# Performance work log

Hardware: AMD Instinct MI355X
Metric: run time of the kernel (lower is better)

Reference implementation:

```python
import jax, jax.numpy as jnp
import numpy as np

B, S, D = 16, 1024, 1024   # batch, n_assets, d_model
H, DK = 16, 64             # num_heads, key_dim (H*DK == D)


def setup_inputs() -> dict:
    key = jax.random.key(0)
    ks = jax.random.split(key, 6)
    scale = 0.02
    return {
        "inputs": jax.random.normal(ks[0], (B, S, D), dtype=jnp.float32),
        "lead_lag_bias": jax.random.normal(ks[1], (S, S), dtype=jnp.float32),
        "Wq": jax.random.normal(ks[2], (D, H * DK), dtype=jnp.float32) * scale,
        "Wk": jax.random.normal(ks[3], (D, H * DK), dtype=jnp.float32) * scale,
        "Wv": jax.random.normal(ks[4], (D, H * DK), dtype=jnp.float32) * scale,
        "Wo": jax.random.normal(ks[5], (H * DK, D), dtype=jnp.float32) * scale,
        "bias_transform": jnp.ones((H,), dtype=jnp.float32),
    }


def reference(inputs, lead_lag_bias, Wq, Wk, Wv, Wo, bias_transform):
    # inputs: [B, S, D]; lead_lag_bias: [S, S]
    inv_sqrt_dk = 1.0 / np.sqrt(DK)
    q = (inputs @ Wq).reshape(B, S, H, DK).transpose(0, 2, 1, 3)  # [B,H,S,Dk]
    k = (inputs @ Wk).reshape(B, S, H, DK).transpose(0, 2, 1, 3)
    v = (inputs @ Wv).reshape(B, S, H, DK).transpose(0, 2, 1, 3)
    scores = jnp.einsum('bhqd,bhkd->bhqk', q, k) * inv_sqrt_dk  # [B,H,S,S]
    # per-head scaled static lead-lag bias (broadcast over batch)
    scores = scores + bias_transform[None, :, None, None] * lead_lag_bias[None, None, :, :]
    attn = jax.nn.softmax(scores, axis=-1)
    out = jnp.einsum('bhqk,bhkd->bhqd', attn, v)  # [B,H,S,Dk]
    out = out.transpose(0, 2, 1, 3).reshape(B, S, H * DK)
    return out @ Wo  # [B, S, D]
```

## Files before the change

### kernel.cpp

```cpp
#include <hip/hip_runtime.h>

typedef __attribute__((ext_vector_type(4))) float f32x4;
typedef __attribute__((ext_vector_type(8))) __bf16 bf16x8;
typedef __attribute__((ext_vector_type(8))) unsigned short u16x8;
typedef __attribute__((ext_vector_type(2))) unsigned int u32x2;

#define MFMA16(a, b, c) \
  __builtin_amdgcn_mfma_f32_16x16x32_bf16(__builtin_bit_cast(bf16x8, (a)), \
                                          __builtin_bit_cast(bf16x8, (b)), (c), 0, 0, 0)

__device__ __forceinline__ unsigned short f2bf(float f) {
  unsigned int u = __builtin_bit_cast(unsigned int, f);
  u += 0x7FFFu + ((u >> 16) & 1u);
  return (unsigned short)(u >> 16);
}

__device__ __forceinline__ unsigned int packbf(float lo, float hi) {
  return (unsigned int)f2bf(lo) | ((unsigned int)f2bf(hi) << 16);
}

__device__ __forceinline__ void gload16(const void* g, void* l) {
  __builtin_amdgcn_global_load_lds(
      (const __attribute__((address_space(1))) void*)g,
      (__attribute__((address_space(3))) void*)l, 16, 0, 0);
}

__global__ __launch_bounds__(256) void xconv(
    const float* __restrict__ X, unsigned short* __restrict__ Xb)
{
  size_t i = ((size_t)blockIdx.x * 256 + threadIdx.x) * 8;
  f32x4 f0 = *(const f32x4*)(X + i);
  f32x4 f1 = *(const f32x4*)(X + i + 4);
  u16x8 v;
  v[0] = f2bf(f0[0]); v[1] = f2bf(f0[1]); v[2] = f2bf(f0[2]); v[3] = f2bf(f0[3]);
  v[4] = f2bf(f1[0]); v[5] = f2bf(f1[1]); v[6] = f2bf(f1[2]); v[7] = f2bf(f1[3]);
  *(u16x8*)(Xb + i) = v;
}

__global__ __launch_bounds__(256) void wtrans(
    const float* __restrict__ Wq, const float* __restrict__ Wk,
    const float* __restrict__ Wv, const float* __restrict__ Wo,
    unsigned short* __restrict__ Wt)
{
  __shared__ unsigned short tile[32][33];
  const int z = blockIdx.z;
  const float* W = (z == 0) ? Wq : (z == 1) ? Wk : (z == 2) ? Wv : Wo;
  unsigned short* T = Wt + (size_t)z * 1024 * 1024;
  const int tx = threadIdx.x, ty = threadIdx.y;
  const int x = blockIdx.x * 32 + tx;
  const int y0 = blockIdx.y * 32;
#pragma unroll
  for (int i = 0; i < 4; ++i)
    tile[ty + i * 8][tx] = f2bf(W[(size_t)(y0 + ty + i * 8) * 1024 + x]);
  __syncthreads();
#pragma unroll
  for (int i = 0; i < 4; ++i)
    T[(size_t)(blockIdx.x * 32 + ty + i * 8) * 1024 + y0 + tx] = tile[tx][ty + i * 8];
}

__global__ __launch_bounds__(256) void qkv_gemm(
    const unsigned short* __restrict__ Xb, const unsigned short* __restrict__ Wt,
    unsigned short* __restrict__ Qo, unsigned short* __restrict__ Ko,
    unsigned short* __restrict__ Vo)
{
  const int bx = blockIdx.x;
  const int z = bx >> 3;
  const int bn = (bx & 7) * 128;
  const int bm = blockIdx.y * 128;
  const unsigned short* Wz = Wt + (size_t)z * 1024 * 1024;
  unsigned short* Out = (z == 0) ? Qo : (z == 1) ? Ko : Vo;

  const int tid = threadIdx.x;
  const int w = tid >> 6, l = tid & 63, l15 = l & 15, lg = l >> 4;
  const int wr = w >> 1, wc = w & 1;

  __shared__ alignas(16) unsigned short sA[128][32];
  __shared__ alignas(16) unsigned short sB[128][32];

  const int srow = w * 32 + (l >> 2);
  const int scol = (l & 3) * 8;
  const unsigned short* gA = Xb + (size_t)(bm + srow) * 1024 + scol;
  const unsigned short* gB = Wz + (size_t)(bn + srow) * 1024 + scol;
  unsigned short* lA = &sA[srow][scol];
  unsigned short* lB = &sB[srow][scol];

  f32x4 acc[4][4];
  const f32x4 zero = {0.f, 0.f, 0.f, 0.f};
#pragma unroll
  for (int i = 0; i < 4; ++i)
#pragma unroll
    for (int j = 0; j < 4; ++j) acc[i][j] = zero;

  for (int k0 = 0; k0 < 1024; k0 += 32) {
    __syncthreads();
#pragma unroll
    for (int p = 0; p < 2; ++p) {
      gload16(gA + (size_t)p * 16 * 1024 + k0, lA + p * 16 * 32);
      gload16(gB + (size_t)p * 16 * 1024 + k0, lB + p * 16 * 32);
    }
    __syncthreads();

    u16x8 af[4], bf[4];
#pragma unroll
    for (int m = 0; m < 4; ++m)
      af[m] = *(const u16x8*)&sA[wr * 64 + m * 16 + l15][lg * 8];
#pragma unroll
    for (int n = 0; n < 4; ++n)
      bf[n] = *(const u16x8*)&sB[wc * 64 + n * 16 + l15][lg * 8];
#pragma unroll
    for (int m = 0; m < 4; ++m)
#pragma unroll
      for (int n = 0; n < 4; ++n)
        acc[m][n] = MFMA16(af[m], bf[n], acc[m][n]);
  }

#pragma unroll
  for (int m = 0; m < 4; ++m) {
    int grow_b = bm + wr * 64 + m * 16 + lg * 4;
#pragma unroll
    for (int n = 0; n < 4; ++n) {
      int gcol = bn + wc * 64 + n * 16 + l15;
      int hh = gcol >> 6, dk = gcol & 63;
#pragma unroll
      for (int t = 0; t < 4; ++t) {
        int grow = grow_b + t;
        int bb = grow >> 10, s = grow & 1023;
        Out[(((size_t)(bb * 16 + hh)) * 1024 + s) * 64 + dk] = f2bf(acc[m][n][t]);
      }
    }
  }
}

__global__ __launch_bounds__(256) void vtrans(
    const unsigned short* __restrict__ V, unsigned short* __restrict__ Vt)
{
  __shared__ unsigned short tile[64 * 64];
  const int s0 = blockIdx.x * 64;
  const size_t bh = (size_t)blockIdx.y * (64 * 1024);
  const int tid = threadIdx.x;

#pragma unroll
  for (int p = 0; p < 2; ++p) {
    int id = p * 256 + tid;
    int s = id >> 3, cc = id & 7;
    u16x8 v = *(const u16x8*)(V + bh + (size_t)(s0 + s) * 64 + cc * 8);
    *(u16x8*)&tile[s * 64 + ((cc ^ (s >> 3)) * 8)] = v;
  }
  __syncthreads();
#pragma unroll
  for (int p = 0; p < 2; ++p) {
    int id = p * 256 + tid;
    int d = id >> 3, sc = id & 7;
    u16x8 v;
#pragma unroll
    for (int i = 0; i < 8; ++i)
      v[i] = tile[(sc * 8 + i) * 64 + (((d >> 3) ^ sc) * 8) + (d & 7)];
    *(u16x8*)(Vt + bh + (size_t)d * 1024 + s0 + sc * 8) = v;
  }
}

__global__ __launch_bounds__(256) void attn(
    const unsigned short* __restrict__ Q, const unsigned short* __restrict__ Kg,
    const unsigned short* __restrict__ Vtg, const float* __restrict__ LL,
    const float* __restrict__ btr, unsigned short* __restrict__ O)
{
  const int q0 = blockIdx.x * 64;
  const int h = blockIdx.y, b = blockIdx.z;
  const int tid = threadIdx.x;
  const int w = tid >> 6, l = tid & 63, l15 = l & 15, lg = l >> 4;

  __shared__ alignas(16) unsigned short sK[64 * 64];
  __shared__ alignas(16) unsigned short sVt[64 * 64];
  __shared__ alignas(16) unsigned short sP[4][16 * 64];

  const float bt = btr[h];
  const size_t bh = (size_t)(b * 16 + h) * (1024 * 64);
  const unsigned short* Qb = Q + bh;
  const unsigned short* Kp = Kg + bh;
  const unsigned short* Vp = Vtg + bh;

  u16x8 qf[2];
  {
    const unsigned short* qp = Qb + (size_t)(q0 + w * 16 + l15) * 64 + lg * 8;
    qf[0] = *(const u16x8*)qp;
    qf[1] = *(const u16x8*)(qp + 32);
  }
  const int qrow = q0 + w * 16 + l15;

  float mrow = -1e30f, lrow = 0.f;
  f32x4 o[4];
  const f32x4 zero = {0.f, 0.f, 0.f, 0.f};
#pragma unroll
  for (int dn = 0; dn < 4; ++dn) o[dn] = zero;

  const int srow0 = tid >> 3, scc = tid & 7;

  for (int kt = 0; kt < 16; ++kt) {
    __syncthreads();
#pragma unroll
    for (int p = 0; p < 2; ++p) {
      int row = p * 32 + srow0;
      u16x8 vk = *(const u16x8*)(Kp + (size_t)(kt * 64 + row) * 64 + scc * 8);
      u16x8 vv = *(const u16x8*)(Vp + (size_t)row * 1024 + kt * 64 + scc * 8);
      *(u16x8*)&sK[row * 64 + ((scc ^ (row & 7)) * 8)] = vk;
      *(u16x8*)&sVt[row * 64 + ((scc ^ (row & 7)) * 8)] = vv;
    }
    __syncthreads();

    f32x4 llv[4];
#pragma unroll
    for (int jn = 0; jn < 4; ++jn)
      llv[jn] = *(const f32x4*)(LL + (size_t)qrow * 1024 + kt * 64 + jn * 16 + lg * 4);

    f32x4 s[4];
#pragma unroll
    for (int jn = 0; jn < 4; ++jn) s[jn] = zero;
#pragma unroll
    for (int dc = 0; dc < 2; ++dc) {
#pragma unroll
      for (int jn = 0; jn < 4; ++jn) {
        int row = jn * 16 + l15;
        u16x8 kfr = *(const u16x8*)&sK[row * 64 + (((dc * 4 + lg) ^ (row & 7)) * 8)];
        s[jn] = MFMA16(kfr, qf[dc], s[jn]);
      }
    }

#pragma unroll
    for (int jn = 0; jn < 4; ++jn)
#pragma unroll
      for (int t = 0; t < 4; ++t)
        s[jn][t] = s[jn][t] * 0.125f + bt * llv[jn][t];

    float tm = s[0][0];
#pragma unroll
    for (int jn = 0; jn < 4; ++jn)
#pragma unroll
      for (int t = 0; t < 4; ++t) tm = fmaxf(tm, s[jn][t]);
    tm = fmaxf(tm, __shfl_xor(tm, 16, 64));
    tm = fmaxf(tm, __shfl_xor(tm, 32, 64));
    float mn = fmaxf(mrow, tm);
    float sc = __expf(mrow - mn);
    mrow = mn;

    float rs = 0.f;
    unsigned int pk[4][2];
#pragma unroll
    for (int jn = 0; jn < 4; ++jn) {
      float p0 = __expf(s[jn][0] - mn);
      float p1 = __expf(s[jn][1] - mn);
      float p2 = __expf(s[jn][2] - mn);
      float p3 = __expf(s[jn][3] - mn);
      rs += (p0 + p1) + (p2 + p3);
      pk[jn][0] = packbf(p0, p1);
      pk[jn][1] = packbf(p2, p3);
    }
    rs += __shfl_xor(rs, 16, 64);
    rs += __shfl_xor(rs, 32, 64);
    lrow = lrow * sc + rs;
#pragma unroll
    for (int dn = 0; dn < 4; ++dn) o[dn] *= sc;

#pragma unroll
    for (int jn = 0; jn < 4; ++jn) {
      int elem = l15 * 64 + (((jn * 2 + (lg >> 1)) ^ (l15 & 7)) * 8) + (lg & 1) * 4;
      u32x2 v2; v2[0] = pk[jn][0]; v2[1] = pk[jn][1];
      *(u32x2*)&sP[w][elem] = v2;
    }

#pragma unroll
    for (int kc = 0; kc < 2; ++kc) {
      u16x8 pb = *(const u16x8*)&sP[w][l15 * 64 + (((kc * 4 + lg) ^ (l15 & 7)) * 8)];
#pragma unroll
      for (int dn = 0; dn < 4; ++dn) {
        int vr = dn * 16 + l15;
        u16x8 vfr = *(const u16x8*)&sVt[vr * 64 + (((kc * 4 + lg) ^ (vr & 7)) * 8)];
        o[dn] = MFMA16(vfr, pb, o[dn]);
      }
    }
  }

  float inv = 1.f / lrow;
  unsigned short* Op = O + ((size_t)(b * 1024 + qrow)) * 1024 + h * 64;
#pragma unroll
  for (int dn = 0; dn < 4; ++dn) {
    u32x2 v2;
    v2[0] = packbf(o[dn][0] * inv, o[dn][1] * inv);
    v2[1] = packbf(o[dn][2] * inv, o[dn][3] * inv);
    *(u32x2*)(Op + dn * 16 + lg * 4) = v2;
  }
}

__global__ __launch_bounds__(256) void out_gemm(
    const unsigned short* __restrict__ A, const unsigned short* __restrict__ Bt,
    float* __restrict__ C)
{
  const int bn = blockIdx.x * 128;
  const int bm = blockIdx.y * 128;
  const int tid = threadIdx.x;
  const int w = tid >> 6, l = tid & 63, l15 = l & 15, lg = l >> 4;
  const int wr = w >> 1, wc = w & 1;

  __shared__ alignas(16) unsigned short sA[128][32];
  __shared__ alignas(16) unsigned short sB[128][32];

  const int srow = w * 32 + (l >> 2);
  const int scol = (l & 3) * 8;
  const unsigned short* gA = A + (size_t)(bm + srow) * 1024 + scol;
  const unsigned short* gB = Bt + (size_t)(bn + srow) * 1024 + scol;
  unsigned short* lA = &sA[srow][scol];
  unsigned short* lB = &sB[srow][scol];

  f32x4 acc[4][4];
  const f32x4 zero = {0.f, 0.f, 0.f, 0.f};
#pragma unroll
  for (int i = 0; i < 4; ++i)
#pragma unroll
    for (int j = 0; j < 4; ++j) acc[i][j] = zero;

  for (int k0 = 0; k0 < 1024; k0 += 32) {
    __syncthreads();
#pragma unroll
    for (int p = 0; p < 2; ++p) {
      gload16(gA + (size_t)p * 16 * 1024 + k0, lA + p * 16 * 32);
      gload16(gB + (size_t)p * 16 * 1024 + k0, lB + p * 16 * 32);
    }
    __syncthreads();

    u16x8 af[4], bf[4];
#pragma unroll
    for (int m = 0; m < 4; ++m)
      af[m] = *(const u16x8*)&sA[wr * 64 + m * 16 + l15][lg * 8];
#pragma unroll
    for (int n = 0; n < 4; ++n)
      bf[n] = *(const u16x8*)&sB[wc * 64 + n * 16 + l15][lg * 8];
#pragma unroll
    for (int m = 0; m < 4; ++m)
#pragma unroll
      for (int n = 0; n < 4; ++n)
        acc[m][n] = MFMA16(af[m], bf[n], acc[m][n]);
  }

#pragma unroll
  for (int m = 0; m < 4; ++m) {
    int grow_b = bm + wr * 64 + m * 16 + lg * 4;
#pragma unroll
    for (int n = 0; n < 4; ++n) {
      int gcol = bn + wc * 64 + n * 16 + l15;
#pragma unroll
      for (int t = 0; t < 4; ++t)
        C[(size_t)(grow_b + t) * 1024 + gcol] = acc[m][n][t];
    }
  }
}

extern "C" void kernel_launch(void* const* d_in, const int* in_sizes, int n_in,
                              void* d_out, int out_size, void* d_ws, size_t ws_size,
                              hipStream_t stream) {
  const float* X  = (const float*)d_in[0];
  const float* LL = (const float*)d_in[1];
  const float* Wq = (const float*)d_in[2];
  const float* Wk = (const float*)d_in[3];
  const float* Wv = (const float*)d_in[4];
  const float* Wo = (const float*)d_in[5];
  const float* bt = (const float*)d_in[6];
  float* out = (float*)d_out;

  unsigned short* ws = (unsigned short*)d_ws;
  const size_t QKV = (size_t)16 * 16 * 1024 * 64;
  unsigned short* Qb = ws;
  unsigned short* Kb = Qb + QKV;
  unsigned short* Vb = Kb + QKV;
  unsigned short* Vt = Vb + QKV;
  unsigned short* Wt = Vt + QKV;
  unsigned short* Ob = Vb;
  unsigned short* Xbb = Vt;

  xconv<<<dim3(8192), 256, 0, stream>>>(X, Xbb);
  wtrans<<<dim3(32, 32, 4), dim3(32, 8), 0, stream>>>(Wq, Wk, Wv, Wo, Wt);
  qkv_gemm<<<dim3(24, 128), 256, 0, stream>>>(Xbb, Wt, Qb, Kb, Vb);
  vtrans<<<dim3(16, 256), 256, 0, stream>>>(Vb, Vt);
  attn<<<dim3(16, 16, 16), 256, 0, stream>>>(Qb, Kb, Vt, LL, bt, Ob);
  out_gemm<<<dim3(8, 128), 256, 0, stream>>>(Ob, Wt + 3 * 1024 * 1024, out);
}
```

Before: 506.5 us.

## Load K/V fragments directly from global and add lazy softmax rescaling

```diff
diff --git a/kernel.cpp b/kernel.cpp
--- a/kernel.cpp
+++ b/kernel.cpp
@@ -2,6 +2,7 @@
 
 typedef __attribute__((ext_vector_type(4))) float f32x4;
 typedef __attribute__((ext_vector_type(8))) __bf16 bf16x8;
+typedef __attribute__((ext_vector_type(2))) __bf16 bf16x2;
 typedef __attribute__((ext_vector_type(8))) unsigned short u16x8;
 typedef __attribute__((ext_vector_type(2))) unsigned int u32x2;
 
@@ -15,8 +16,11 @@
   return (unsigned short)(u >> 16);
 }
 
-__device__ __forceinline__ unsigned int packbf(float lo, float hi) {
-  return (unsigned int)f2bf(lo) | ((unsigned int)f2bf(hi) << 16);
+__device__ __forceinline__ unsigned int packbf2(float lo, float hi) {
+  bf16x2 v;
+  v[0] = (__bf16)lo;
+  v[1] = (__bf16)hi;
+  return __builtin_bit_cast(unsigned int, v);
 }
 
 __device__ __forceinline__ void gload16(const void* g, void* l) {
@@ -169,114 +173,119 @@
   const int tid = threadIdx.x;
   const int w = tid >> 6, l = tid & 63, l15 = l & 15, lg = l >> 4;
 
-  __shared__ alignas(16) unsigned short sK[64 * 64];
-  __shared__ alignas(16) unsigned short sVt[64 * 64];
   __shared__ alignas(16) unsigned short sP[4][16 * 64];
 
   const float bt = btr[h];
   const size_t bh = (size_t)(b * 16 + h) * (1024 * 64);
-  const unsigned short* Qb = Q + bh;
-  const unsigned short* Kp = Kg + bh;
-  const unsigned short* Vp = Vtg + bh;
 
   u16x8 qf[2];
   {
-    const unsigned short* qp = Qb + (size_t)(q0 + w * 16 + l15) * 64 + lg * 8;
+    const unsigned short* qp = Q + bh + (size_t)(q0 + w * 16 + l15) * 64 + lg * 8;
     qf[0] = *(const u16x8*)qp;
     qf[1] = *(const u16x8*)(qp + 32);
   }
   const int qrow = q0 + w * 16 + l15;
 
-  float mrow = -1e30f, lrow = 0.f;
+  const unsigned short* kA[4];
+#pragma unroll
+  for (int jn = 0; jn < 4; ++jn)
+    kA[jn] = Kg + bh + (size_t)(jn * 16 + l15) * 64 + lg * 8;
+  const unsigned short* vA[4];
+#pragma unroll
+  for (int dn = 0; dn < 4; ++dn)
+    vA[dn] = Vtg + bh + (size_t)(dn * 16 + l15) * 1024 + lg * 8;
+
+  unsigned short* sPw = &sP[w][0];
+  int wr_off[4];
+#pragma unroll
+  for (int jn = 0; jn < 4; ++jn)
+    wr_off[jn] = l15 * 64 + (((jn * 2 + (lg >> 1)) ^ (l15 & 7)) * 8) + (lg & 1) * 4;
+  int rd_off[2];
+#pragma unroll
+  for (int kc = 0; kc < 2; ++kc)
+    rd_off[kc] = l15 * 64 + (((kc * 4 + lg) ^ (l15 & 7)) * 8);
+
+  const float* llp = LL + (size_t)qrow * 1024 + lg * 4;
+
+  float mrow = -3e38f, lrow = 0.f;
   f32x4 o[4];
   const f32x4 zero = {0.f, 0.f, 0.f, 0.f};
 #pragma unroll
   for (int dn = 0; dn < 4; ++dn) o[dn] = zero;
 
-  const int srow0 = tid >> 3, scc = tid & 7;
+  const float L2E = 1.44269504f;
 
   for (int kt = 0; kt < 16; ++kt) {
-    __syncthreads();
-#pragma unroll
-    for (int p = 0; p < 2; ++p) {
-      int row = p * 32 + srow0;
-      u16x8 vk = *(const u16x8*)(Kp + (size_t)(kt * 64 + row) * 64 + scc * 8);
-      u16x8 vv = *(const u16x8*)(Vp + (size_t)row * 1024 + kt * 64 + scc * 8);
-      *(u16x8*)&sK[row * 64 + ((scc ^ (row & 7)) * 8)] = vk;
-      *(u16x8*)&sVt[row * 64 + ((scc ^ (row & 7)) * 8)] = vv;
-    }
-    __syncthreads();
-
-    f32x4 llv[4];
-#pragma unroll
-    for (int jn = 0; jn < 4; ++jn)
-      llv[jn] = *(const f32x4*)(LL + (size_t)qrow * 1024 + kt * 64 + jn * 16 + lg * 4);
-
-    f32x4 s[4];
-#pragma unroll
-    for (int jn = 0; jn < 4; ++jn) s[jn] = zero;
+    f32x4 s4[4];
+#pragma unroll
+    for (int jn = 0; jn < 4; ++jn) s4[jn] = zero;
 #pragma unroll
     for (int dc = 0; dc < 2; ++dc) {
 #pragma unroll
       for (int jn = 0; jn < 4; ++jn) {
-        int row = jn * 16 + l15;
-        u16x8 kfr = *(const u16x8*)&sK[row * 64 + (((dc * 4 + lg) ^ (row & 7)) * 8)];
-        s[jn] = MFMA16(kfr, qf[dc], s[jn]);
+        u16x8 kfr = *(const u16x8*)(kA[jn] + dc * 32);
+        s4[jn] = MFMA16(kfr, qf[dc], s4[jn]);
       }
     }
-
-#pragma unroll
-    for (int jn = 0; jn < 4; ++jn)
-#pragma unroll
-      for (int t = 0; t < 4; ++t)
-        s[jn][t] = s[jn][t] * 0.125f + bt * llv[jn][t];
-
-    float tm = s[0][0];
-#pragma unroll
-    for (int jn = 0; jn < 4; ++jn)
-#pragma unroll
-      for (int t = 0; t < 4; ++t) tm = fmaxf(tm, s[jn][t]);
+#pragma unroll
+    for (int jn = 0; jn < 4; ++jn) kA[jn] += 64 * 64;
+
+#pragma unroll
+    for (int jn = 0; jn < 4; ++jn) {
+      f32x4 llv = *(const f32x4*)(llp + jn * 16);
+      s4[jn] = s4[jn] * 0.125f + bt * llv;
+    }
+    llp += 64;
+
+    float tm = fmaxf(fmaxf(s4[0][0], s4[0][1]), fmaxf(s4[0][2], s4[0][3]));
+#pragma unroll
+    for (int jn = 1; jn < 4; ++jn)
+      tm = fmaxf(tm, fmaxf(fmaxf(s4[jn][0], s4[jn][1]), fmaxf(s4[jn][2], s4[jn][3])));
     tm = fmaxf(tm, __shfl_xor(tm, 16, 64));
     tm = fmaxf(tm, __shfl_xor(tm, 32, 64));
-    float mn = fmaxf(mrow, tm);
-    float sc = __expf(mrow - mn);
-    mrow = mn;
-
-    float rs = 0.f;
-    unsigned int pk[4][2];
-#pragma unroll
-    for (int jn = 0; jn < 4; ++jn) {
-      float p0 = __expf(s[jn][0] - mn);
-      float p1 = __expf(s[jn][1] - mn);
-      float p2 = __expf(s[jn][2] - mn);
-      float p3 = __expf(s[jn][3] - mn);
-      rs += (p0 + p1) + (p2 + p3);
-      pk[jn][0] = packbf(p0, p1);
-      pk[jn][1] = packbf(p2, p3);
-    }
+
+    if (__any(tm > mrow + 8.f)) {
+      float mn = fmaxf(mrow, tm);
+      float sc = __expf(mrow - mn);
+      mrow = mn;
+      lrow *= sc;
+#pragma unroll
+      for (int dn = 0; dn < 4; ++dn) o[dn] *= sc;
+    }
+
+    const float mnl = mrow * L2E;
+    f32x4 pv4[4];
+#pragma unroll
+    for (int jn = 0; jn < 4; ++jn)
+#pragma unroll
+      for (int t = 0; t < 4; ++t)
+        pv4[jn][t] = exp2f(s4[jn][t] * L2E - mnl);
+
+    f32x4 a4 = (pv4[0] + pv4[1]) + (pv4[2] + pv4[3]);
+    float rs = (a4[0] + a4[1]) + (a4[2] + a4[3]);
     rs += __shfl_xor(rs, 16, 64);
     rs += __shfl_xor(rs, 32, 64);
-    lrow = lrow * sc + rs;
-#pragma unroll
-    for (int dn = 0; dn < 4; ++dn) o[dn] *= sc;
+    lrow += rs;
 
 #pragma unroll
     for (int jn = 0; jn < 4; ++jn) {
-      int elem = l15 * 64 + (((jn * 2 + (lg >> 1)) ^ (l15 & 7)) * 8) + (lg & 1) * 4;
-      u32x2 v2; v2[0] = pk[jn][0]; v2[1] = pk[jn][1];
-      *(u32x2*)&sP[w][elem] = v2;
+      u32x2 v2;
+      v2[0] = packbf2(pv4[jn][0], pv4[jn][1]);
+      v2[1] = packbf2(pv4[jn][2], pv4[jn][3]);
+      *(u32x2*)&sPw[wr_off[jn]] = v2;
     }
 
 #pragma unroll
     for (int kc = 0; kc < 2; ++kc) {
-      u16x8 pb = *(const u16x8*)&sP[w][l15 * 64 + (((kc * 4 + lg) ^ (l15 & 7)) * 8)];
+      u16x8 pb = *(const u16x8*)&sPw[rd_off[kc]];
 #pragma unroll
       for (int dn = 0; dn < 4; ++dn) {
-        int vr = dn * 16 + l15;
-        u16x8 vfr = *(const u16x8*)&sVt[vr * 64 + (((kc * 4 + lg) ^ (vr & 7)) * 8)];
+        u16x8 vfr = *(const u16x8*)(vA[dn] + kc * 32);
         o[dn] = MFMA16(vfr, pb, o[dn]);
       }
     }
+#pragma unroll
+    for (int dn = 0; dn < 4; ++dn) vA[dn] += 64;
   }
 
   float inv = 1.f / lrow;
@@ -284,8 +293,8 @@
 #pragma unroll
   for (int dn = 0; dn < 4; ++dn) {
     u32x2 v2;
-    v2[0] = packbf(o[dn][0] * inv, o[dn][1] * inv);
-    v2[1] = packbf(o[dn][2] * inv, o[dn][3] * inv);
+    v2[0] = packbf2(o[dn][0] * inv, o[dn][1] * inv);
+    v2[1] = packbf2(o[dn][2] * inv, o[dn][3] * inv);
     *(u32x2*)(Op + dn * 16 + lg * 4) = v2;
   }
 }
```

Measured after the change: 882.3 us. +74.2%, slower.
